# Kernel tuning notes

Hardware: AMD Instinct MI355X
Metric: run time of the kernel (lower is better)

Reference implementation:

```python
import jax, jax.numpy as jnp
import numpy as np

B, L, E, H = 2, 2048, 1024, 16
D = E // H

def setup_inputs() -> dict:
    key = jax.random.key(0)
    ks = jax.random.split(key, 6)
    s = 1.0 / np.sqrt(E)
    return {
        "x": jax.random.normal(ks[0], (B, L, E), dtype=jnp.float32),
        "attention_mask": jnp.ones((B, L), dtype=jnp.float32),
        "Wq": jax.random.normal(ks[1], (E, E), dtype=jnp.float32) * s,
        "Wk": jax.random.normal(ks[2], (E, E), dtype=jnp.float32) * s,
        "Wv": jax.random.normal(ks[3], (E, E), dtype=jnp.float32) * s,
        "Wo": jax.random.normal(ks[4], (E, E), dtype=jnp.float32) * s,
        "bo": jnp.zeros((E,), dtype=jnp.float32),
    }

def reference(x, attention_mask, Wq, Wk, Wv, Wo, bo):
    b, l, e = x.shape
    h, d = H, D

    def proj(W):
        # (B,L,E) @ (E,E)^T -> (B,L,E) -> (B,H,L,D)
        return (x @ W.T).reshape(b, l, h, d).transpose(0, 2, 1, 3)

    q, k, v = proj(Wq), proj(Wk), proj(Wv)

    # multiplicative attention mask on q, k, v (mask shape (B,L) -> (B,1,L,1))
    m = attention_mask[:, None, :, None].astype(x.dtype)
    q, k, v = q * m, k * m, v * m

    scale = 1.0 / np.sqrt(d)
    scores = jnp.einsum('bhqd,bhkd->bhqk', q, k) * scale  # (B,H,L,L)
    causal = jnp.tril(jnp.ones((l, l), dtype=bool))
    scores = jnp.where(causal[None, None], scores, -jnp.inf)
    attn = jax.nn.softmax(scores, axis=-1)
    y = jnp.einsum('bhqk,bhkd->bhqd', attn, v)  # (B,H,L,D)
    y = y.transpose(0, 2, 1, 3).reshape(b, l, e)
    return y @ Wo.T + bo
```

## Files before the change

### kernel.cpp

```cpp
#include <hip/hip_runtime.h>
#include <cstdint>
#include <cstddef>
#include <math.h>

#define BB 2
#define LL 2048
#define EE 1024
#define HH 16
#define DD 64
#define MM (BB*LL)

typedef short short8 __attribute__((ext_vector_type(8)));
typedef float f32x4 __attribute__((ext_vector_type(4)));
typedef float f32x16 __attribute__((ext_vector_type(16)));

#define GPTR __attribute__((address_space(1)))
#define LPTR __attribute__((address_space(3)))

__device__ __forceinline__ unsigned pk_bf16(float lo, float hi) {
  unsigned r;
  asm("v_cvt_pk_bf16_f32 %0, %1, %2" : "=v"(r) : "v"(lo), "v"(hi));
  return r;
}
__device__ __forceinline__ unsigned short f32_bf16(float f) {
  return (unsigned short)pk_bf16(f, f);
}
__device__ __forceinline__ float ex2(float x) {
  float r;
  asm("v_exp_f32 %0, %1" : "=v"(r) : "v"(x));
  return r;
}
__device__ __forceinline__ void swap32(unsigned &a, unsigned &b) {
  asm("v_permlane32_swap_b32 %0, %1" : "+v"(a), "+v"(b));
}
__device__ __forceinline__ float xh_max(float v) {
  union { float f; unsigned u; } a, b;
  a.f = v;
  asm("v_mov_b32 %0, %1" : "=&v"(b.u) : "v"(a.u));
  asm("v_permlane32_swap_b32 %0, %1" : "+v"(a.u), "+v"(b.u));
  return fmaxf(a.f, b.f);
}
__device__ __forceinline__ float xh_sum(float v) {
  union { float f; unsigned u; } a, b;
  a.f = v;
  asm("v_mov_b32 %0, %1" : "=&v"(b.u) : "v"(a.u));
  asm("v_permlane32_swap_b32 %0, %1" : "+v"(a.u), "+v"(b.u));
  return a.f + b.f;
}
__device__ __forceinline__ f32x16 zero16() {
  f32x16 v;
  #pragma unroll
  for (int e = 0; e < 16; ++e) v[e] = 0.f;
  return v;
}

__global__ void cvt_all(const float* __restrict__ x,  const float* __restrict__ wq,
                        const float* __restrict__ wk, const float* __restrict__ wv,
                        const float* __restrict__ wo,
                        unsigned short* __restrict__ xb,  unsigned short* __restrict__ wqb,
                        unsigned short* __restrict__ wkb, unsigned short* __restrict__ wvb,
                        unsigned short* __restrict__ wob)
{
  int i = (blockIdx.x * 256 + threadIdx.x) * 4;
  if (i >= MM * EE + 4 * EE * EE) return;
  const float* s; unsigned short* d; int off;
  if (i < MM * EE) { s = x; d = xb; off = i; }
  else {
    int k = i - MM * EE;
    int w = k >> 20;
    off = k & (EE * EE - 1);
    s = (w == 0) ? wq : (w == 1) ? wk : (w == 2) ? wv : wo;
    d = (w == 0) ? wqb : (w == 1) ? wkb : (w == 2) ? wvb : wob;
  }
  float4 v = *(const float4*)(s + off);
  uint2 o;
  o.x = pk_bf16(v.x, v.y);
  o.y = pk_bf16(v.z, v.w);
  *(uint2*)(d + off) = o;
}

template<int MODE>
__global__ __launch_bounds__(256, 2)
void gemm128(const unsigned short* __restrict__ A,
             const unsigned short* __restrict__ W0,
             const unsigned short* __restrict__ W1,
             const unsigned short* __restrict__ W2,
             const float* __restrict__ mask,
             const float* __restrict__ bias,
             unsigned short* __restrict__ O0,
             unsigned short* __restrict__ O1,
             unsigned short* __restrict__ O2,
             float* __restrict__ OF)
{
  constexpr int K = EE;
  const int tid = threadIdx.x;
  const int lane = tid & 63;
  const int wid = tid >> 6;
  const int g = lane >> 4, li = lane & 15;
  const int m0 = blockIdx.y * 128;
  const int n0 = blockIdx.x * 128;
  const int z = blockIdx.z;

  const unsigned short* Wp = W0;
  if (MODE == 0) Wp = (z == 0) ? W0 : ((z == 1) ? W1 : W2);

  __shared__ unsigned short As[128 * 64];
  __shared__ unsigned short Bs[128 * 64];

  f32x4 acc[4][4];
  f32x4 zero = {0.f, 0.f, 0.f, 0.f};
  #pragma unroll
  for (int i = 0; i < 4; ++i)
    #pragma unroll
    for (int j = 0; j < 4; ++j) acc[i][j] = zero;

  const int wm = (wid >> 1) * 64;
  const int wn = (wid & 1) * 64;

  for (int kt = 0; kt < K; kt += 64) {
    #pragma unroll
    for (int j = 0; j < 4; ++j) {
      int c = j * 256 + tid;
      int row = c >> 3;
      int lcol = ((c & 7) * 16) ^ ((row & 7) << 4);
      __builtin_amdgcn_global_load_lds(
        (const GPTR void*)((const char*)(A + (size_t)(m0 + row) * K + kt) + lcol),
        (LPTR void*)((char*)As + c * 16), 16, 0, 0);
      __builtin_amdgcn_global_load_lds(
        (const GPTR void*)((const char*)(Wp + (size_t)(n0 + row) * K + kt) + lcol),
        (LPTR void*)((char*)Bs + c * 16), 16, 0, 0);
    }
    __syncthreads();

    #pragma unroll
    for (int kk = 0; kk < 2; ++kk) {
      short8 a[4], b[4];
      const int colb = (kk * 32 + g * 8) * 2;
      #pragma unroll
      for (int i = 0; i < 4; ++i) {
        int ar = wm + i * 16 + li;
        a[i] = *(const short8*)((const char*)As + ar * 128 + (colb ^ ((ar & 7) << 4)));
        int br = wn + i * 16 + li;
        b[i] = *(const short8*)((const char*)Bs + br * 128 + (colb ^ ((br & 7) << 4)));
      }
      #pragma unroll
      for (int i = 0; i < 4; ++i)
        #pragma unroll
        for (int j = 0; j < 4; ++j)
          acc[i][j] = __builtin_amdgcn_mfma_f32_16x16x32_bf16(a[i], b[j], acc[i][j], 0, 0, 0);
    }
    __syncthreads();
  }

  if (MODE == 0) {
    if (z == 2) {
      #pragma unroll
      for (int i = 0; i < 4; ++i) {
        int mbase = m0 + wm + i * 16 + g * 4;
        int bb2 = mbase >> 11;
        int l0  = mbase & (LL - 1);
        float mk[4];
        #pragma unroll
        for (int r = 0; r < 4; ++r) mk[r] = mask[mbase + r];
        #pragma unroll
        for (int j = 0; j < 4; ++j) {
          int n = n0 + wn + j * 16 + li;
          int h2 = n >> 6, dd2 = n & 63;
          uint2 o;
          o.x = pk_bf16(acc[i][j][0] * mk[0], acc[i][j][1] * mk[1]);
          o.y = pk_bf16(acc[i][j][2] * mk[2], acc[i][j][3] * mk[3]);
          size_t off = (size_t)(bb2 * HH + h2) * (LL * DD)
                     + (size_t)(l0 >> 5) * (DD * 32) + dd2 * 32 + (l0 & 31);
          *(uint2*)(O2 + off) = o;
        }
      }
    } else {
      unsigned short* Op = (z == 0) ? O0 : O1;
      const float sc = (z == 0) ? 0.125f * 1.44269504088896f : 1.0f;
      #pragma unroll
      for (int i = 0; i < 4; ++i) {
        #pragma unroll
        for (int r = 0; r < 4; ++r) {
          int m = m0 + wm + i * 16 + g * 4 + r;
          float mk = mask[m] * sc;
          int bb = m >> 11;
          int l  = m & (LL - 1);
          #pragma unroll
          for (int j = 0; j < 4; ++j) {
            int n = n0 + wn + j * 16 + li;
            int h = n >> 6, d = n & 63;
            size_t off = (((size_t)(bb * HH + h)) * LL + l) * DD + d;
            Op[off] = f32_bf16(acc[i][j][r] * mk);
          }
        }
      }
    }
  } else {
    #pragma unroll
    for (int i = 0; i < 4; ++i) {
      #pragma unroll
      for (int j = 0; j < 4; ++j) {
        int n = n0 + wn + j * 16 + li;
        float bv = bias[n];
        #pragma unroll
        for (int r = 0; r < 4; ++r) {
          int m = m0 + wm + i * 16 + g * 4 + r;
          OF[(size_t)m * EE + n] = acc[i][j][r] + bv;
        }
      }
    }
  }
}

__global__ __launch_bounds__(128, 2)
void attn11(const unsigned short* __restrict__ Q,
            const unsigned short* __restrict__ K,
            const unsigned short* __restrict__ VT,
            unsigned short* __restrict__ Y)
{
  const int tid = threadIdx.x, lane = tid & 63, w = tid >> 6;
  const int l31 = lane & 31, hi = lane >> 5;

  const int id = blockIdx.x;
  const int lo = id & 7;
  const int r_ = id >> 3;
  const int bh = (r_ & 3) * 8 + lo;
  const int p  = r_ >> 2;
  const int qth = 63 - p;
  const int qtl = p;
  const int b = bh >> 4, h = bh & (HH - 1);
  const size_t kbase = (size_t)bh * LL * DD;

  const unsigned short* Kg  = K + kbase;
  const unsigned short* VTg = VT + kbase;

  const int qrh = qth * 32 + l31;
  const int qrl = qtl * 32 + l31;

  short8 qfh[4], qfl[4];
  {
    const unsigned short* Qr = Q + kbase + (size_t)qrh * DD + hi * 8;
    #pragma unroll
    for (int kc = 0; kc < 4; ++kc) qfh[kc] = *(const short8*)(Qr + kc * 16);
    const unsigned short* Qs = Q + kbase + (size_t)qrl * DD + hi * 8;
    #pragma unroll
    for (int kc = 0; kc < 4; ++kc) qfl[kc] = *(const short8*)(Qs + kc * 16);
  }

  const f32x16 kZero = zero16();
  f32x16 oh0 = zero16(), oh1 = zero16(), ol0 = zero16(), ol1 = zero16();
  float mh = -INFINITY, ml = -INFINITY;
  float lsh4[4] = {0.f, 0.f, 0.f, 0.f};
  float lsl4[4] = {0.f, 0.f, 0.f, 0.f};

  short8 kA[4], vA[4], kB[4], vB[4];

  auto loadtile = [&](short8 (&kk)[4], short8 (&vv)[4], int t2) {
    const int kv0 = t2 << 5;
    const unsigned short* Kp = Kg + ((size_t)(kv0 + l31) << 6) + hi * 8;
    #pragma unroll
    for (int kc = 0; kc < 4; ++kc) kk[kc] = *(const short8*)(Kp + kc * 16);
    const unsigned short* Vp = VTg + (size_t)(kv0 >> 5) * (DD * 32) + l31 * 32 + hi * 8;
    vv[0] = *(const short8*)(Vp);
    vv[1] = *(const short8*)(Vp + 16);
    vv[2] = *(const short8*)(Vp + 32 * 32);
    vv[3] = *(const short8*)(Vp + 32 * 32 + 16);
  };

  loadtile(kA, vA, w);

  auto qk = [&](const short8 (&ck)[4], const short8 (&qf)[4]) -> f32x16 {
    f32x16 s0 = __builtin_amdgcn_mfma_f32_32x32x16_bf16(ck[0], qf[0], kZero, 0, 0, 0);
    f32x16 s1 = __builtin_amdgcn_mfma_f32_32x32x16_bf16(ck[1], qf[1], kZero, 0, 0, 0);
    s0 = __builtin_amdgcn_mfma_f32_32x32x16_bf16(ck[2], qf[2], s0, 0, 0, 0);
    s1 = __builtin_amdgcn_mfma_f32_32x32x16_bf16(ck[3], qf[3], s1, 0, 0, 0);
    #pragma unroll
    for (int e = 0; e < 16; ++e) s0[e] += s1[e];
    return s0;
  };

  auto diagmask = [&](f32x16 &s) {
    #pragma unroll
    for (int i = 0; i < 16; ++i) {
      int kvr = (i & 3) + 8 * (i >> 2) + 4 * hi;
      if (kvr > l31) s[i] = -INFINITY;
    }
  };

  auto process = [&](f32x16 &s, const short8 (&cv)[4],
                     float &mq, float (&ls4)[4], f32x16 &o0, f32x16 &o1) {
    float r0 = fmaxf(fmaxf(fmaxf(s[0], s[8]),  fmaxf(s[1], s[9])),  fmaxf(s[2], s[10]));
    float r1 = fmaxf(fmaxf(fmaxf(s[3], s[11]), fmaxf(s[4], s[12])), fmaxf(s[5], s[13]));
    float r2 = fmaxf(fmaxf(s[6], s[14]), fmaxf(s[7], s[15]));
    float mv = fmaxf(fmaxf(r0, r1), r2);

    if (!__all(mv <= mq + 8.0f)) {
      float mnew = fmaxf(mq, xh_max(mv));
      float al = ex2(mq - mnew);
      mq = mnew;
      #pragma unroll
      for (int e = 0; e < 16; ++e) { o0[e] *= al; o1[e] *= al; }
      #pragma unroll
      for (int e = 0; e < 4; ++e) ls4[e] *= al;
    }

    #pragma unroll
    for (int e = 0; e < 16; ++e) s[e] = ex2(s[e] - mq);
    ls4[0] += (s[0] + s[8])  + (s[4] + s[12]);
    ls4[1] += (s[1] + s[9])  + (s[5] + s[13]);
    ls4[2] += (s[2] + s[10]) + (s[6] + s[14]);
    ls4[3] += (s[3] + s[11]) + (s[7] + s[15]);

    auto mkfrag = [&](int base) -> short8 {
      unsigned a0 = pk_bf16(s[base + 0], s[base + 1]);
      unsigned a1 = pk_bf16(s[base + 2], s[base + 3]);
      unsigned b0 = pk_bf16(s[base + 4], s[base + 5]);
      unsigned b1 = pk_bf16(s[base + 6], s[base + 7]);
      swap32(a0, b0);
      swap32(a1, b1);
      union { unsigned u[4]; short8 s8; } f;
      f.u[0] = a0; f.u[1] = a1; f.u[2] = b0; f.u[3] = b1;
      return f.s8;
    };
    short8 pf0 = mkfrag(0), pf1 = mkfrag(8);

    o0 = __builtin_amdgcn_mfma_f32_32x32x16_bf16(cv[0], pf0, o0, 0, 0, 0);
    o1 = __builtin_amdgcn_mfma_f32_32x32x16_bf16(cv[2], pf0, o1, 0, 0, 0);
    o0 = __builtin_amdgcn_mfma_f32_32x32x16_bf16(cv[1], pf1, o0, 0, 0, 0);
    o1 = __builtin_amdgcn_mfma_f32_32x32x16_bf16(cv[3], pf1, o1, 0, 0, 0);
  };

  auto body = [&](short8 (&ck)[4], short8 (&cv)[4],
                  short8 (&nk)[4], short8 (&nv)[4], int t) {
    if (t + 2 <= qth) loadtile(nk, nv, t + 2);

    if (t <= qtl) {
      f32x16 sh = qk(ck, qfh);
      f32x16 sl = qk(ck, qfl);
      if (t == qtl) diagmask(sl);
      process(sh, cv, mh, lsh4, oh0, oh1);
      process(sl, cv, ml, lsl4, ol0, ol1);
    } else {
      f32x16 sh = qk(ck, qfh);
      if (t == qth) diagmask(sh);
      process(sh, cv, mh, lsh4, oh0, oh1);
    }
  };

  for (int t = w; t <= qth; t += 4) {
    body(kA, vA, kB, vB, t);
    if (t + 2 <= qth) body(kB, vB, kA, vA, t + 2);
  }

  float lsh = (lsh4[0] + lsh4[1]) + (lsh4[2] + lsh4[3]);
  float lsl = (lsl4[0] + lsl4[1]) + (lsl4[2] + lsl4[3]);

  __shared__ float mg[2][64][34];
  if (w == 1) {
    mg[0][lane][0] = mh; mg[0][lane][1] = lsh;
    mg[1][lane][0] = ml; mg[1][lane][1] = lsl;
    #pragma unroll
    for (int e = 0; e < 16; ++e) {
      mg[0][lane][2 + e] = oh0[e]; mg[0][lane][18 + e] = oh1[e];
      mg[1][lane][2 + e] = ol0[e]; mg[1][lane][18 + e] = ol1[e];
    }
  }
  __syncthreads();
  if (w == 0) {
    #pragma unroll
    for (int q = 0; q < 2; ++q) {
      float mw = (q == 0) ? mh : ml;
      float lw = (q == 0) ? lsh : lsl;
      const f32x16& o0 = (q == 0) ? oh0 : ol0;
      const f32x16& o1 = (q == 0) ? oh1 : ol1;
      int qrow = (q == 0) ? qrh : qrl;
      float m1 = mg[q][lane][0], l1 = mg[q][lane][1];
      float M = fmaxf(mw, m1);
      float a0 = ex2(fmaxf(mw - M, -200.0f));
      float a1 = ex2(fmaxf(m1 - M, -200.0f));
      float LtH = lw * a0 + l1 * a1;
      float Lt = xh_sum(LtH);
      float inv = 1.0f / Lt;
      unsigned short* Yr = Y + ((size_t)b * LL + qrow) * EE + h * DD;
      #pragma unroll
      for (int rg = 0; rg < 4; ++rg) {
        uint2 u0, u1;
        int i = rg * 4;
        u0.x = pk_bf16((o0[i]     * a0 + mg[q][lane][2 + i]     * a1) * inv,
                       (o0[i + 1] * a0 + mg[q][lane][3 + i]     * a1) * inv);
        u0.y = pk_bf16((o0[i + 2] * a0 + mg[q][lane][4 + i]     * a1) * inv,
                       (o0[i + 3] * a0 + mg[q][lane][5 + i]     * a1) * inv);
        u1.x = pk_bf16((o1[i]     * a0 + mg[q][lane][18 + i]    * a1) * inv,
                       (o1[i + 1] * a0 + mg[q][lane][19 + i]    * a1) * inv);
        u1.y = pk_bf16((o1[i + 2] * a0 + mg[q][lane][20 + i]    * a1) * inv,
                       (o1[i + 3] * a0 + mg[q][lane][21 + i]    * a1) * inv);
        *(uint2*)(Yr + rg * 8 + hi * 4) = u0;
        *(uint2*)(Yr + 32 + rg * 8 + hi * 4) = u1;
      }
    }
  }
}

extern "C" void kernel_launch(void* const* d_in, const int* in_sizes, int n_in,
                              void* d_out, int out_size, void* d_ws, size_t ws_size,
                              hipStream_t stream) {
  const float* x    = (const float*)d_in[0];
  const float* mask = (const float*)d_in[1];
  const float* Wq   = (const float*)d_in[2];
  const float* Wk   = (const float*)d_in[3];
  const float* Wv   = (const float*)d_in[4];
  const float* Wo   = (const float*)d_in[5];
  const float* bo   = (const float*)d_in[6];
  float* out = (float*)d_out;

  char* ws = (char*)d_ws;
  unsigned short* xb  = (unsigned short*)(ws);
  unsigned short* wqb = (unsigned short*)(ws + ((size_t)8  << 20));
  unsigned short* wkb = (unsigned short*)(ws + ((size_t)10 << 20));
  unsigned short* wvb = (unsigned short*)(ws + ((size_t)12 << 20));
  unsigned short* wob = (unsigned short*)(ws + ((size_t)14 << 20));
  unsigned short* Qb  = (unsigned short*)(ws + ((size_t)16 << 20));
  unsigned short* Kb  = (unsigned short*)(ws + ((size_t)24 << 20));
  unsigned short* VTb = (unsigned short*)(ws + ((size_t)32 << 20));
  unsigned short* Yb  = (unsigned short*)(ws + ((size_t)40 << 20));

  cvt_all<<<8192, 256, 0, stream>>>(x, Wq, Wk, Wv, Wo, xb, wqb, wkb, wvb, wob);

  gemm128<0><<<dim3(EE / 128, MM / 128, 3), 256, 0, stream>>>(
      xb, wqb, wkb, wvb, mask, nullptr, Qb, Kb, VTb, nullptr);

  attn11<<<dim3(1024), 128, 0, stream>>>(Qb, Kb, VTb, Yb);

  gemm128<1><<<dim3(EE / 128, MM / 128, 1), 256, 0, stream>>>(
      Yb, wob, nullptr, nullptr, nullptr, bo, nullptr, nullptr, nullptr, out);
}
```

Measured before the change: 107.5 us.

## Restructure attention loop with split accumulators and paired softmax rescale

The attention kernel's KV loop is restructured so the high query tile keeps two independent online-softmax accumulators, one for even tiles and one for odd tiles. They are merged at the end. Two score tiles are processed together with a single combined rescale vote, and the next tile loads are issued after the current tile is consumed rather than before. The QK product now uses one serial MFMA chain instead of two partial chains plus an add. The aim is more instruction-level parallelism and fewer divergent rescale branches, at the cost of more registers (extra accumulators) and a serial MFMA dependency chain.

```diff
diff --git a/kernel.cpp b/kernel.cpp
--- a/kernel.cpp
+++ b/kernel.cpp
@@ -213,7 +213,7 @@
 }
 
 __global__ __launch_bounds__(128, 2)
-void attn11(const unsigned short* __restrict__ Q,
+void attn12(const unsigned short* __restrict__ Q,
             const unsigned short* __restrict__ K,
             const unsigned short* __restrict__ VT,
             unsigned short* __restrict__ Y)
@@ -247,13 +247,13 @@
     for (int kc = 0; kc < 4; ++kc) qfl[kc] = *(const short8*)(Qs + kc * 16);
   }
 
-  const f32x16 kZero = zero16();
-  f32x16 oh0 = zero16(), oh1 = zero16(), ol0 = zero16(), ol1 = zero16();
-  float mh = -INFINITY, ml = -INFINITY;
-  float lsh4[4] = {0.f, 0.f, 0.f, 0.f};
-  float lsl4[4] = {0.f, 0.f, 0.f, 0.f};
-
-  short8 kA[4], vA[4], kB[4], vB[4];
+  f32x16 oE0 = zero16(), oE1 = zero16();
+  f32x16 oO0 = zero16(), oO1 = zero16();
+  f32x16 oL0 = zero16(), oL1 = zero16();
+  float mE = -INFINITY, mO = -INFINITY, mL = -INFINITY;
+  float lsE0 = 0.f, lsE1 = 0.f, lsO0 = 0.f, lsO1 = 0.f, lsL0 = 0.f, lsL1 = 0.f;
+
+  short8 kE[4], vE[4], kO[4], vO[4];
 
   auto loadtile = [&](short8 (&kk)[4], short8 (&vv)[4], int t2) {
     const int kv0 = t2 << 5;
@@ -267,16 +267,12 @@
     vv[3] = *(const short8*)(Vp + 32 * 32 + 16);
   };
 
-  loadtile(kA, vA, w);
-
-  auto qk = [&](const short8 (&ck)[4], const short8 (&qf)[4]) -> f32x16 {
-    f32x16 s0 = __builtin_amdgcn_mfma_f32_32x32x16_bf16(ck[0], qf[0], kZero, 0, 0, 0);
-    f32x16 s1 = __builtin_amdgcn_mfma_f32_32x32x16_bf16(ck[1], qf[1], kZero, 0, 0, 0);
-    s0 = __builtin_amdgcn_mfma_f32_32x32x16_bf16(ck[2], qf[2], s0, 0, 0, 0);
-    s1 = __builtin_amdgcn_mfma_f32_32x32x16_bf16(ck[3], qf[3], s1, 0, 0, 0);
-    #pragma unroll
-    for (int e = 0; e < 16; ++e) s0[e] += s1[e];
-    return s0;
+  auto qk4 = [&](const short8 (&ck)[4], const short8 (&qf)[4]) -> f32x16 {
+    f32x16 s = __builtin_amdgcn_mfma_f32_32x32x16_bf16(ck[0], qf[0], zero16(), 0, 0, 0);
+    s = __builtin_amdgcn_mfma_f32_32x32x16_bf16(ck[1], qf[1], s, 0, 0, 0);
+    s = __builtin_amdgcn_mfma_f32_32x32x16_bf16(ck[2], qf[2], s, 0, 0, 0);
+    s = __builtin_amdgcn_mfma_f32_32x32x16_bf16(ck[3], qf[3], s, 0, 0, 0);
+    return s;
   };
 
   auto diagmask = [&](f32x16 &s) {
@@ -287,92 +283,151 @@
     }
   };
 
-  auto process = [&](f32x16 &s, const short8 (&cv)[4],
-                     float &mq, float (&ls4)[4], f32x16 &o0, f32x16 &o1) {
+  auto localmax = [&](const f32x16 &s) -> float {
     float r0 = fmaxf(fmaxf(fmaxf(s[0], s[8]),  fmaxf(s[1], s[9])),  fmaxf(s[2], s[10]));
     float r1 = fmaxf(fmaxf(fmaxf(s[3], s[11]), fmaxf(s[4], s[12])), fmaxf(s[5], s[13]));
     float r2 = fmaxf(fmaxf(s[6], s[14]), fmaxf(s[7], s[15]));
-    float mv = fmaxf(fmaxf(r0, r1), r2);
-
-    if (!__all(mv <= mq + 8.0f)) {
-      float mnew = fmaxf(mq, xh_max(mv));
-      float al = ex2(mq - mnew);
-      mq = mnew;
-      #pragma unroll
-      for (int e = 0; e < 16; ++e) { o0[e] *= al; o1[e] *= al; }
-      #pragma unroll
-      for (int e = 0; e < 4; ++e) ls4[e] *= al;
-    }
-
+    return fmaxf(fmaxf(r0, r1), r2);
+  };
+
+  auto mkfrag = [&](const f32x16 &s, int base) -> short8 {
+    unsigned a0 = pk_bf16(s[base + 0], s[base + 1]);
+    unsigned a1 = pk_bf16(s[base + 2], s[base + 3]);
+    unsigned b0 = pk_bf16(s[base + 4], s[base + 5]);
+    unsigned b1 = pk_bf16(s[base + 6], s[base + 7]);
+    swap32(a0, b0);
+    swap32(a1, b1);
+    union { unsigned u[4]; short8 s8; } f;
+    f.u[0] = a0; f.u[1] = a1; f.u[2] = b0; f.u[3] = b1;
+    return f.s8;
+  };
+
+  auto tail = [&](f32x16 &s, float mq, float &l0, float &l1,
+                  const short8 (&cv)[4], f32x16 &o0, f32x16 &o1) {
     #pragma unroll
     for (int e = 0; e < 16; ++e) s[e] = ex2(s[e] - mq);
-    ls4[0] += (s[0] + s[8])  + (s[4] + s[12]);
-    ls4[1] += (s[1] + s[9])  + (s[5] + s[13]);
-    ls4[2] += (s[2] + s[10]) + (s[6] + s[14]);
-    ls4[3] += (s[3] + s[11]) + (s[7] + s[15]);
-
-    auto mkfrag = [&](int base) -> short8 {
-      unsigned a0 = pk_bf16(s[base + 0], s[base + 1]);
-      unsigned a1 = pk_bf16(s[base + 2], s[base + 3]);
-      unsigned b0 = pk_bf16(s[base + 4], s[base + 5]);
-      unsigned b1 = pk_bf16(s[base + 6], s[base + 7]);
-      swap32(a0, b0);
-      swap32(a1, b1);
-      union { unsigned u[4]; short8 s8; } f;
-      f.u[0] = a0; f.u[1] = a1; f.u[2] = b0; f.u[3] = b1;
-      return f.s8;
-    };
-    short8 pf0 = mkfrag(0), pf1 = mkfrag(8);
-
+    l0 += (s[0] + s[8])  + (s[4] + s[12]) + (s[1] + s[9])  + (s[5] + s[13]);
+    l1 += (s[2] + s[10]) + (s[6] + s[14]) + (s[3] + s[11]) + (s[7] + s[15]);
+    short8 pf0 = mkfrag(s, 0), pf1 = mkfrag(s, 8);
     o0 = __builtin_amdgcn_mfma_f32_32x32x16_bf16(cv[0], pf0, o0, 0, 0, 0);
     o1 = __builtin_amdgcn_mfma_f32_32x32x16_bf16(cv[2], pf0, o1, 0, 0, 0);
     o0 = __builtin_amdgcn_mfma_f32_32x32x16_bf16(cv[1], pf1, o0, 0, 0, 0);
     o1 = __builtin_amdgcn_mfma_f32_32x32x16_bf16(cv[3], pf1, o1, 0, 0, 0);
   };
 
-  auto body = [&](short8 (&ck)[4], short8 (&cv)[4],
-                  short8 (&nk)[4], short8 (&nv)[4], int t) {
-    if (t + 2 <= qth) loadtile(nk, nv, t + 2);
-
+  auto pp = [&](f32x16 &sA, float &mA, float &lA0, float &lA1,
+                const short8 (&cvA)[4], f32x16 &a0, f32x16 &a1,
+                f32x16 &sB, float &mB, float &lB0, float &lB1,
+                const short8 (&cvB)[4], f32x16 &b0, f32x16 &b1) {
+    float mvA = localmax(sA);
+    float mvB = localmax(sB);
+    if (!__all(fmaxf(mvA - mA, mvB - mB) <= 8.0f)) {
+      float mnA = fmaxf(mA, xh_max(mvA));
+      float alA = ex2(mA - mnA);
+      mA = mnA; lA0 *= alA; lA1 *= alA;
+      #pragma unroll
+      for (int e = 0; e < 16; ++e) { a0[e] *= alA; a1[e] *= alA; }
+      float mnB = fmaxf(mB, xh_max(mvB));
+      float alB = ex2(mB - mnB);
+      mB = mnB; lB0 *= alB; lB1 *= alB;
+      #pragma unroll
+      for (int e = 0; e < 16; ++e) { b0[e] *= alB; b1[e] *= alB; }
+    }
+    tail(sA, mA, lA0, lA1, cvA, a0, a1);
+    tail(sB, mB, lB0, lB1, cvB, b0, b1);
+  };
+
+  auto ps = [&](f32x16 &s, float &mq, float &l0, float &l1,
+                const short8 (&cv)[4], f32x16 &o0, f32x16 &o1) {
+    float mv = localmax(s);
+    if (!__all(mv <= mq + 8.0f)) {
+      float mn = fmaxf(mq, xh_max(mv));
+      float al = ex2(mq - mn);
+      mq = mn; l0 *= al; l1 *= al;
+      #pragma unroll
+      for (int e = 0; e < 16; ++e) { o0[e] *= al; o1[e] *= al; }
+    }
+    tail(s, mq, l0, l1, cv, o0, o1);
+  };
+
+  loadtile(kE, vE, w);
+  loadtile(kO, vO, w + 2);
+
+  int t = w;
+  while (t + 2 <= qth) {
+    const bool shE = (t <= qtl), shO = (t + 2 <= qtl);
+    if (shE) {
+      f32x16 sE = qk4(kE, qfh);
+      f32x16 sL = qk4(kE, qfl);
+      if (t == qtl) diagmask(sL);
+      pp(sE, mE, lsE0, lsE1, vE, oE0, oE1,
+         sL, mL, lsL0, lsL1, vE, oL0, oL1);
+      if (t + 4 <= qth) loadtile(kE, vE, t + 4);
+      f32x16 sO = qk4(kO, qfh);
+      if (shO) {
+        f32x16 sL2 = qk4(kO, qfl);
+        if (t + 2 == qtl) diagmask(sL2);
+        pp(sO, mO, lsO0, lsO1, vO, oO0, oO1,
+           sL2, mL, lsL0, lsL1, vO, oL0, oL1);
+      } else {
+        if (t + 2 == qth) diagmask(sO);
+        ps(sO, mO, lsO0, lsO1, vO, oO0, oO1);
+      }
+      if (t + 6 <= qth) loadtile(kO, vO, t + 6);
+    } else {
+      f32x16 sE = qk4(kE, qfh);
+      f32x16 sO = qk4(kO, qfh);
+      if (t + 2 == qth) diagmask(sO);
+      pp(sE, mE, lsE0, lsE1, vE, oE0, oE1,
+         sO, mO, lsO0, lsO1, vO, oO0, oO1);
+      if (t + 4 <= qth) loadtile(kE, vE, t + 4);
+      if (t + 6 <= qth) loadtile(kO, vO, t + 6);
+    }
+    t += 4;
+  }
+  if (t <= qth) {
+    f32x16 sE = qk4(kE, qfh);
+    if (t == qth) diagmask(sE);
     if (t <= qtl) {
-      f32x16 sh = qk(ck, qfh);
-      f32x16 sl = qk(ck, qfl);
-      if (t == qtl) diagmask(sl);
-      process(sh, cv, mh, lsh4, oh0, oh1);
-      process(sl, cv, ml, lsl4, ol0, ol1);
+      f32x16 sL = qk4(kE, qfl);
+      if (t == qtl) diagmask(sL);
+      pp(sE, mE, lsE0, lsE1, vE, oE0, oE1,
+         sL, mL, lsL0, lsL1, vE, oL0, oL1);
     } else {
-      f32x16 sh = qk(ck, qfh);
-      if (t == qth) diagmask(sh);
-      process(sh, cv, mh, lsh4, oh0, oh1);
-    }
-  };
-
-  for (int t = w; t <= qth; t += 4) {
-    body(kA, vA, kB, vB, t);
-    if (t + 2 <= qth) body(kB, vB, kA, vA, t + 2);
-  }
-
-  float lsh = (lsh4[0] + lsh4[1]) + (lsh4[2] + lsh4[3]);
-  float lsl = (lsl4[0] + lsl4[1]) + (lsl4[2] + lsl4[3]);
+      ps(sE, mE, lsE0, lsE1, vE, oE0, oE1);
+    }
+  }
+
+  float mH = fmaxf(mE, mO);
+  float aE = ex2(fmaxf(mE - mH, -200.0f));
+  float aO = ex2(fmaxf(mO - mH, -200.0f));
+  float lsH = (lsE0 + lsE1) * aE + (lsO0 + lsO1) * aO;
+  f32x16 oh0, oh1;
+  #pragma unroll
+  for (int e = 0; e < 16; ++e) {
+    oh0[e] = oE0[e] * aE + oO0[e] * aO;
+    oh1[e] = oE1[e] * aE + oO1[e] * aO;
+  }
+  float lsL = lsL0 + lsL1;
 
   __shared__ float mg[2][64][34];
   if (w == 1) {
-    mg[0][lane][0] = mh; mg[0][lane][1] = lsh;
-    mg[1][lane][0] = ml; mg[1][lane][1] = lsl;
+    mg[0][lane][0] = mH; mg[0][lane][1] = lsH;
+    mg[1][lane][0] = mL; mg[1][lane][1] = lsL;
     #pragma unroll
     for (int e = 0; e < 16; ++e) {
       mg[0][lane][2 + e] = oh0[e]; mg[0][lane][18 + e] = oh1[e];
-      mg[1][lane][2 + e] = ol0[e]; mg[1][lane][18 + e] = ol1[e];
+      mg[1][lane][2 + e] = oL0[e]; mg[1][lane][18 + e] = oL1[e];
     }
   }
   __syncthreads();
   if (w == 0) {
     #pragma unroll
     for (int q = 0; q < 2; ++q) {
-      float mw = (q == 0) ? mh : ml;
-      float lw = (q == 0) ? lsh : lsl;
-      const f32x16& o0 = (q == 0) ? oh0 : ol0;
-      const f32x16& o1 = (q == 0) ? oh1 : ol1;
+      float mw = (q == 0) ? mH : mL;
+      float lw = (q == 0) ? lsH : lsL;
+      const f32x16& o0 = (q == 0) ? oh0 : oL0;
+      const f32x16& o1 = (q == 0) ? oh1 : oL1;
       int qrow = (q == 0) ? qrh : qrl;
       float m1 = mg[q][lane][0], l1 = mg[q][lane][1];
       float M = fmaxf(mw, m1);
@@ -386,14 +441,14 @@
       for (int rg = 0; rg < 4; ++rg) {
         uint2 u0, u1;
         int i = rg * 4;
-        u0.x = pk_bf16((o0[i]     * a0 + mg[q][lane][2 + i]     * a1) * inv,
-                       (o0[i + 1] * a0 + mg[q][lane][3 + i]     * a1) * inv);
-        u0.y = pk_bf16((o0[i + 2] * a0 + mg[q][lane][4 + i]     * a1) * inv,
-                       (o0[i + 3] * a0 + mg[q][lane][5 + i]     * a1) * inv);
-        u1.x = pk_bf16((o1[i]     * a0 + mg[q][lane][18 + i]    * a1) * inv,
-                       (o1[i + 1] * a0 + mg[q][lane][19 + i]    * a1) * inv);
-        u1.y = pk_bf16((o1[i + 2] * a0 + mg[q][lane][20 + i]    * a1) * inv,
-                       (o1[i + 3] * a0 + mg[q][lane][21 + i]    * a1) * inv);
+        u0.x = pk_bf16((o0[i]     * a0 + mg[q][lane][2 + i]  * a1) * inv,
+                       (o0[i + 1] * a0 + mg[q][lane][3 + i]  * a1) * inv);
+        u0.y = pk_bf16((o0[i + 2] * a0 + mg[q][lane][4 + i]  * a1) * inv,
+                       (o0[i + 3] * a0 + mg[q][lane][5 + i]  * a1) * inv);
+        u1.x = pk_bf16((o1[i]     * a0 + mg[q][lane][18 + i] * a1) * inv,
+                       (o1[i + 1] * a0 + mg[q][lane][19 + i] * a1) * inv);
+        u1.y = pk_bf16((o1[i + 2] * a0 + mg[q][lane][20 + i] * a1) * inv,
+                       (o1[i + 3] * a0 + mg[q][lane][21 + i] * a1) * inv);
         *(uint2*)(Yr + rg * 8 + hi * 4) = u0;
         *(uint2*)(Yr + 32 + rg * 8 + hi * 4) = u1;
       }
@@ -429,7 +484,7 @@
   gemm128<0><<<dim3(EE / 128, MM / 128, 3), 256, 0, stream>>>(
       xb, wqb, wkb, wvb, mask, nullptr, Qb, Kb, VTb, nullptr);
 
-  attn11<<<dim3(1024), 128, 0, stream>>>(Qb, Kb, VTb, Yb);
+  attn12<<<dim3(1024), 128, 0, stream>>>(Qb, Kb, VTb, Yb);
 
   gemm128<1><<<dim3(EE / 128, MM / 128, 1), 256, 0, stream>>>(
       Yb, wob, nullptr, nullptr, nullptr, bo, nullptr, nullptr, nullptr, out);
```

After: 112.4 us. 4.6% more time.

## Double-buffer LDS tiles in projection GEMMs and flatten QKV grid

Applied to the files above, without the earlier changes.

The projection GEMM now ping-pongs between two LDS buffers. The next K-tile's global-to-LDS loads are issued before the MFMAs on the current tile, so load latency overlaps compute and one barrier per iteration is removed. The QKV launch becomes a flat 2D grid that treats the contiguous Wq/Wk/Wv bf16 copies as a single 3072-row weight matrix and derives the output selector from n0. LDS use per block doubles to 64KB, which may limit occupancy. The merged grid depends on the three weight buffers staying adjacent in the workspace.

```diff
diff --git a/kernel.cpp b/kernel.cpp
--- a/kernel.cpp
+++ b/kernel.cpp
@@ -81,16 +81,14 @@
 
 template<int MODE>
 __global__ __launch_bounds__(256, 2)
-void gemm128(const unsigned short* __restrict__ A,
-             const unsigned short* __restrict__ W0,
-             const unsigned short* __restrict__ W1,
-             const unsigned short* __restrict__ W2,
-             const float* __restrict__ mask,
-             const float* __restrict__ bias,
-             unsigned short* __restrict__ O0,
-             unsigned short* __restrict__ O1,
-             unsigned short* __restrict__ O2,
-             float* __restrict__ OF)
+void gemm2p(const unsigned short* __restrict__ A,
+            const unsigned short* __restrict__ W,
+            const float* __restrict__ mask,
+            const float* __restrict__ bias,
+            unsigned short* __restrict__ O0,
+            unsigned short* __restrict__ O1,
+            unsigned short* __restrict__ O2,
+            float* __restrict__ OF)
 {
   constexpr int K = EE;
   const int tid = threadIdx.x;
@@ -99,13 +97,9 @@
   const int g = lane >> 4, li = lane & 15;
   const int m0 = blockIdx.y * 128;
   const int n0 = blockIdx.x * 128;
-  const int z = blockIdx.z;
-
-  const unsigned short* Wp = W0;
-  if (MODE == 0) Wp = (z == 0) ? W0 : ((z == 1) ? W1 : W2);
-
-  __shared__ unsigned short As[128 * 64];
-  __shared__ unsigned short Bs[128 * 64];
+
+  __shared__ unsigned short As[2][128 * 64];
+  __shared__ unsigned short Bs[2][128 * 64];
 
   f32x4 acc[4][4];
   f32x4 zero = {0.f, 0.f, 0.f, 0.f};
@@ -117,7 +111,7 @@
   const int wm = (wid >> 1) * 64;
   const int wn = (wid & 1) * 64;
 
-  for (int kt = 0; kt < K; kt += 64) {
+  auto stage = [&](int buf, int kt) {
     #pragma unroll
     for (int j = 0; j < 4; ++j) {
       int c = j * 256 + tid;
@@ -125,12 +119,20 @@
       int lcol = ((c & 7) * 16) ^ ((row & 7) << 4);
       __builtin_amdgcn_global_load_lds(
         (const GPTR void*)((const char*)(A + (size_t)(m0 + row) * K + kt) + lcol),
-        (LPTR void*)((char*)As + c * 16), 16, 0, 0);
+        (LPTR void*)((char*)As[buf] + c * 16), 16, 0, 0);
       __builtin_amdgcn_global_load_lds(
-        (const GPTR void*)((const char*)(Wp + (size_t)(n0 + row) * K + kt) + lcol),
-        (LPTR void*)((char*)Bs + c * 16), 16, 0, 0);
-    }
-    __syncthreads();
+        (const GPTR void*)((const char*)(W + (size_t)(n0 + row) * K + kt) + lcol),
+        (LPTR void*)((char*)Bs[buf] + c * 16), 16, 0, 0);
+    }
+  };
+
+  stage(0, 0);
+  asm volatile("s_waitcnt vmcnt(0)" ::: "memory");
+  __builtin_amdgcn_s_barrier();
+
+  int cur = 0;
+  for (int kt = 0; kt < K; kt += 64) {
+    if (kt + 64 < K) stage(cur ^ 1, kt + 64);
 
     #pragma unroll
     for (int kk = 0; kk < 2; ++kk) {
@@ -139,9 +141,9 @@
       #pragma unroll
       for (int i = 0; i < 4; ++i) {
         int ar = wm + i * 16 + li;
-        a[i] = *(const short8*)((const char*)As + ar * 128 + (colb ^ ((ar & 7) << 4)));
+        a[i] = *(const short8*)((const char*)As[cur] + ar * 128 + (colb ^ ((ar & 7) << 4)));
         int br = wn + i * 16 + li;
-        b[i] = *(const short8*)((const char*)Bs + br * 128 + (colb ^ ((br & 7) << 4)));
+        b[i] = *(const short8*)((const char*)Bs[cur] + br * 128 + (colb ^ ((br & 7) << 4)));
       }
       #pragma unroll
       for (int i = 0; i < 4; ++i)
@@ -149,10 +151,16 @@
         for (int j = 0; j < 4; ++j)
           acc[i][j] = __builtin_amdgcn_mfma_f32_16x16x32_bf16(a[i], b[j], acc[i][j], 0, 0, 0);
     }
-    __syncthreads();
+
+    if (kt + 64 < K) {
+      asm volatile("s_waitcnt vmcnt(0) lgkmcnt(0)" ::: "memory");
+      __builtin_amdgcn_s_barrier();
+      cur ^= 1;
+    }
   }
 
   if (MODE == 0) {
+    const int z = n0 >> 10;
     if (z == 2) {
       #pragma unroll
       for (int i = 0; i < 4; ++i) {
@@ -164,7 +172,7 @@
         for (int r = 0; r < 4; ++r) mk[r] = mask[mbase + r];
         #pragma unroll
         for (int j = 0; j < 4; ++j) {
-          int n = n0 + wn + j * 16 + li;
+          int n = (n0 & 1023) + wn + j * 16 + li;
           int h2 = n >> 6, dd2 = n & 63;
           uint2 o;
           o.x = pk_bf16(acc[i][j][0] * mk[0], acc[i][j][1] * mk[1]);
@@ -187,7 +195,7 @@
           int l  = m & (LL - 1);
           #pragma unroll
           for (int j = 0; j < 4; ++j) {
-            int n = n0 + wn + j * 16 + li;
+            int n = (n0 & 1023) + wn + j * 16 + li;
             int h = n >> 6, d = n & 63;
             size_t off = (((size_t)(bb * HH + h)) * LL + l) * DD + d;
             Op[off] = f32_bf16(acc[i][j][r] * mk);
@@ -426,11 +434,11 @@
 
   cvt_all<<<8192, 256, 0, stream>>>(x, Wq, Wk, Wv, Wo, xb, wqb, wkb, wvb, wob);
 
-  gemm128<0><<<dim3(EE / 128, MM / 128, 3), 256, 0, stream>>>(
-      xb, wqb, wkb, wvb, mask, nullptr, Qb, Kb, VTb, nullptr);
+  gemm2p<0><<<dim3(3 * EE / 128, MM / 128), 256, 0, stream>>>(
+      xb, wqb, mask, nullptr, Qb, Kb, VTb, nullptr);
 
   attn11<<<dim3(1024), 128, 0, stream>>>(Qb, Kb, VTb, Yb);
 
-  gemm128<1><<<dim3(EE / 128, MM / 128, 1), 256, 0, stream>>>(
-      Yb, wob, nullptr, nullptr, nullptr, bo, nullptr, nullptr, nullptr, out);
-}
+  gemm2p<1><<<dim3(EE / 128, MM / 128), 256, 0, stream>>>(
+      Yb, wob, nullptr, bo, nullptr, nullptr, nullptr, out);
+}
```

Measured after the change: 115.0 us. 7.0% more time.

## Split paired query tiles into one tile per block with higher occupancy

Applied to the files above, without the earlier changes.

The attention kernel used to handle a heavy and a light causal query tile per block, with a double-buffered K/V register prefetch. Now each block processes a single query tile, the grid doubles to 2048 blocks, and launch bounds allow 4 blocks per CU. The aim is to cut register pressure and rely on occupancy rather than explicit prefetch to hide memory latency. In exchange it drops the software prefetch and the K/V reuse across the two tiles, so K/V loads double and the causal workload becomes uneven across blocks, with heavy tiles scheduled first.

```diff
diff --git a/kernel.cpp b/kernel.cpp
--- a/kernel.cpp
+++ b/kernel.cpp
@@ -212,8 +212,8 @@
   }
 }
 
-__global__ __launch_bounds__(128, 2)
-void attn11(const unsigned short* __restrict__ Q,
+__global__ __launch_bounds__(128, 4)
+void attn13(const unsigned short* __restrict__ Q,
             const unsigned short* __restrict__ K,
             const unsigned short* __restrict__ VT,
             unsigned short* __restrict__ Y)
@@ -225,70 +225,61 @@
   const int lo = id & 7;
   const int r_ = id >> 3;
   const int bh = (r_ & 3) * 8 + lo;
-  const int p  = r_ >> 2;
-  const int qth = 63 - p;
-  const int qtl = p;
+  const int qt = 63 - (r_ >> 2);
   const int b = bh >> 4, h = bh & (HH - 1);
   const size_t kbase = (size_t)bh * LL * DD;
 
   const unsigned short* Kg  = K + kbase;
   const unsigned short* VTg = VT + kbase;
 
-  const int qrh = qth * 32 + l31;
-  const int qrl = qtl * 32 + l31;
-
-  short8 qfh[4], qfl[4];
+  const int qrow = qt * 32 + l31;
+
+  short8 qf[4];
   {
-    const unsigned short* Qr = Q + kbase + (size_t)qrh * DD + hi * 8;
-    #pragma unroll
-    for (int kc = 0; kc < 4; ++kc) qfh[kc] = *(const short8*)(Qr + kc * 16);
-    const unsigned short* Qs = Q + kbase + (size_t)qrl * DD + hi * 8;
-    #pragma unroll
-    for (int kc = 0; kc < 4; ++kc) qfl[kc] = *(const short8*)(Qs + kc * 16);
+    const unsigned short* Qr = Q + kbase + (size_t)qrow * DD + hi * 8;
+    #pragma unroll
+    for (int kc = 0; kc < 4; ++kc) qf[kc] = *(const short8*)(Qr + kc * 16);
   }
 
   const f32x16 kZero = zero16();
-  f32x16 oh0 = zero16(), oh1 = zero16(), ol0 = zero16(), ol1 = zero16();
-  float mh = -INFINITY, ml = -INFINITY;
-  float lsh4[4] = {0.f, 0.f, 0.f, 0.f};
-  float lsl4[4] = {0.f, 0.f, 0.f, 0.f};
-
-  short8 kA[4], vA[4], kB[4], vB[4];
-
-  auto loadtile = [&](short8 (&kk)[4], short8 (&vv)[4], int t2) {
-    const int kv0 = t2 << 5;
-    const unsigned short* Kp = Kg + ((size_t)(kv0 + l31) << 6) + hi * 8;
-    #pragma unroll
-    for (int kc = 0; kc < 4; ++kc) kk[kc] = *(const short8*)(Kp + kc * 16);
-    const unsigned short* Vp = VTg + (size_t)(kv0 >> 5) * (DD * 32) + l31 * 32 + hi * 8;
-    vv[0] = *(const short8*)(Vp);
-    vv[1] = *(const short8*)(Vp + 16);
-    vv[2] = *(const short8*)(Vp + 32 * 32);
-    vv[3] = *(const short8*)(Vp + 32 * 32 + 16);
-  };
-
-  loadtile(kA, vA, w);
-
-  auto qk = [&](const short8 (&ck)[4], const short8 (&qf)[4]) -> f32x16 {
-    f32x16 s0 = __builtin_amdgcn_mfma_f32_32x32x16_bf16(ck[0], qf[0], kZero, 0, 0, 0);
-    f32x16 s1 = __builtin_amdgcn_mfma_f32_32x32x16_bf16(ck[1], qf[1], kZero, 0, 0, 0);
-    s0 = __builtin_amdgcn_mfma_f32_32x32x16_bf16(ck[2], qf[2], s0, 0, 0, 0);
-    s1 = __builtin_amdgcn_mfma_f32_32x32x16_bf16(ck[3], qf[3], s1, 0, 0, 0);
-    #pragma unroll
-    for (int e = 0; e < 16; ++e) s0[e] += s1[e];
-    return s0;
-  };
-
-  auto diagmask = [&](f32x16 &s) {
-    #pragma unroll
-    for (int i = 0; i < 16; ++i) {
-      int kvr = (i & 3) + 8 * (i >> 2) + 4 * hi;
-      if (kvr > l31) s[i] = -INFINITY;
-    }
-  };
-
-  auto process = [&](f32x16 &s, const short8 (&cv)[4],
-                     float &mq, float (&ls4)[4], f32x16 &o0, f32x16 &o1) {
+  f32x16 o0 = zero16(), o1 = zero16();
+  float mq = -INFINITY;
+  float ls4[4] = {0.f, 0.f, 0.f, 0.f};
+
+  short8 kA[4], vA[4];
+
+  for (int t = w; t <= qt; t += 2) {
+    {
+      const int kv0 = t << 5;
+      const unsigned short* Kp = Kg + ((size_t)(kv0 + l31) << 6) + hi * 8;
+      #pragma unroll
+      for (int kc = 0; kc < 4; ++kc) kA[kc] = *(const short8*)(Kp + kc * 16);
+      const unsigned short* Vp = VTg + (size_t)(kv0 >> 5) * (DD * 32) + l31 * 32 + hi * 8;
+      vA[0] = *(const short8*)(Vp);
+      vA[1] = *(const short8*)(Vp + 16);
+      vA[2] = *(const short8*)(Vp + 32 * 32);
+      vA[3] = *(const short8*)(Vp + 32 * 32 + 16);
+    }
+
+    f32x16 s;
+    {
+      f32x16 s0 = __builtin_amdgcn_mfma_f32_32x32x16_bf16(kA[0], qf[0], kZero, 0, 0, 0);
+      f32x16 s1 = __builtin_amdgcn_mfma_f32_32x32x16_bf16(kA[1], qf[1], kZero, 0, 0, 0);
+      s0 = __builtin_amdgcn_mfma_f32_32x32x16_bf16(kA[2], qf[2], s0, 0, 0, 0);
+      s1 = __builtin_amdgcn_mfma_f32_32x32x16_bf16(kA[3], qf[3], s1, 0, 0, 0);
+      #pragma unroll
+      for (int e = 0; e < 16; ++e) s0[e] += s1[e];
+      s = s0;
+    }
+
+    if (t == qt) {
+      #pragma unroll
+      for (int i = 0; i < 16; ++i) {
+        int kvr = (i & 3) + 8 * (i >> 2) + 4 * hi;
+        if (kvr > l31) s[i] = -INFINITY;
+      }
+    }
+
     float r0 = fmaxf(fmaxf(fmaxf(s[0], s[8]),  fmaxf(s[1], s[9])),  fmaxf(s[2], s[10]));
     float r1 = fmaxf(fmaxf(fmaxf(s[3], s[11]), fmaxf(s[4], s[12])), fmaxf(s[5], s[13]));
     float r2 = fmaxf(fmaxf(s[6], s[14]), fmaxf(s[7], s[15]));
@@ -324,79 +315,46 @@
     };
     short8 pf0 = mkfrag(0), pf1 = mkfrag(8);
 
-    o0 = __builtin_amdgcn_mfma_f32_32x32x16_bf16(cv[0], pf0, o0, 0, 0, 0);
-    o1 = __builtin_amdgcn_mfma_f32_32x32x16_bf16(cv[2], pf0, o1, 0, 0, 0);
-    o0 = __builtin_amdgcn_mfma_f32_32x32x16_bf16(cv[1], pf1, o0, 0, 0, 0);
-    o1 = __builtin_amdgcn_mfma_f32_32x32x16_bf16(cv[3], pf1, o1, 0, 0, 0);
-  };
-
-  auto body = [&](short8 (&ck)[4], short8 (&cv)[4],
-                  short8 (&nk)[4], short8 (&nv)[4], int t) {
-    if (t + 2 <= qth) loadtile(nk, nv, t + 2);
-
-    if (t <= qtl) {
-      f32x16 sh = qk(ck, qfh);
-      f32x16 sl = qk(ck, qfl);
-      if (t == qtl) diagmask(sl);
-      process(sh, cv, mh, lsh4, oh0, oh1);
-      process(sl, cv, ml, lsl4, ol0, ol1);
-    } else {
-      f32x16 sh = qk(ck, qfh);
-      if (t == qth) diagmask(sh);
-      process(sh, cv, mh, lsh4, oh0, oh1);
-    }
-  };
-
-  for (int t = w; t <= qth; t += 4) {
-    body(kA, vA, kB, vB, t);
-    if (t + 2 <= qth) body(kB, vB, kA, vA, t + 2);
-  }
-
-  float lsh = (lsh4[0] + lsh4[1]) + (lsh4[2] + lsh4[3]);
-  float lsl = (lsl4[0] + lsl4[1]) + (lsl4[2] + lsl4[3]);
-
-  __shared__ float mg[2][64][34];
+    o0 = __builtin_amdgcn_mfma_f32_32x32x16_bf16(vA[0], pf0, o0, 0, 0, 0);
+    o1 = __builtin_amdgcn_mfma_f32_32x32x16_bf16(vA[2], pf0, o1, 0, 0, 0);
+    o0 = __builtin_amdgcn_mfma_f32_32x32x16_bf16(vA[1], pf1, o0, 0, 0, 0);
+    o1 = __builtin_amdgcn_mfma_f32_32x32x16_bf16(vA[3], pf1, o1, 0, 0, 0);
+  }
+
+  float lq = (ls4[0] + ls4[1]) + (ls4[2] + ls4[3]);
+
+  __shared__ float mg[64][34];
   if (w == 1) {
-    mg[0][lane][0] = mh; mg[0][lane][1] = lsh;
-    mg[1][lane][0] = ml; mg[1][lane][1] = lsl;
+    mg[lane][0] = mq; mg[lane][1] = lq;
     #pragma unroll
     for (int e = 0; e < 16; ++e) {
-      mg[0][lane][2 + e] = oh0[e]; mg[0][lane][18 + e] = oh1[e];
-      mg[1][lane][2 + e] = ol0[e]; mg[1][lane][18 + e] = ol1[e];
+      mg[lane][2 + e] = o0[e]; mg[lane][18 + e] = o1[e];
     }
   }
   __syncthreads();
   if (w == 0) {
-    #pragma unroll
-    for (int q = 0; q < 2; ++q) {
-      float mw = (q == 0) ? mh : ml;
-      float lw = (q == 0) ? lsh : lsl;
-      const f32x16& o0 = (q == 0) ? oh0 : ol0;
-      const f32x16& o1 = (q == 0) ? oh1 : ol1;
-      int qrow = (q == 0) ? qrh : qrl;
-      float m1 = mg[q][lane][0], l1 = mg[q][lane][1];
-      float M = fmaxf(mw, m1);
-      float a0 = ex2(fmaxf(mw - M, -200.0f));
-      float a1 = ex2(fmaxf(m1 - M, -200.0f));
-      float LtH = lw * a0 + l1 * a1;
-      float Lt = xh_sum(LtH);
-      float inv = 1.0f / Lt;
-      unsigned short* Yr = Y + ((size_t)b * LL + qrow) * EE + h * DD;
-      #pragma unroll
-      for (int rg = 0; rg < 4; ++rg) {
-        uint2 u0, u1;
-        int i = rg * 4;
-        u0.x = pk_bf16((o0[i]     * a0 + mg[q][lane][2 + i]     * a1) * inv,
-                       (o0[i + 1] * a0 + mg[q][lane][3 + i]     * a1) * inv);
-        u0.y = pk_bf16((o0[i + 2] * a0 + mg[q][lane][4 + i]     * a1) * inv,
-                       (o0[i + 3] * a0 + mg[q][lane][5 + i]     * a1) * inv);
-        u1.x = pk_bf16((o1[i]     * a0 + mg[q][lane][18 + i]    * a1) * inv,
-                       (o1[i + 1] * a0 + mg[q][lane][19 + i]    * a1) * inv);
-        u1.y = pk_bf16((o1[i + 2] * a0 + mg[q][lane][20 + i]    * a1) * inv,
-                       (o1[i + 3] * a0 + mg[q][lane][21 + i]    * a1) * inv);
-        *(uint2*)(Yr + rg * 8 + hi * 4) = u0;
-        *(uint2*)(Yr + 32 + rg * 8 + hi * 4) = u1;
-      }
+    float m1 = mg[lane][0], l1 = mg[lane][1];
+    float M = fmaxf(mq, m1);
+    float a0 = ex2(fmaxf(mq - M, -200.0f));
+    float a1 = ex2(fmaxf(m1 - M, -200.0f));
+    float LtH = lq * a0 + l1 * a1;
+    float Lt = xh_sum(LtH);
+    float inv = 1.0f / Lt;
+    unsigned short* Yr = Y + ((size_t)b * LL + qrow) * EE + h * DD;
+    #pragma unroll
+    for (int rg = 0; rg < 4; ++rg) {
+      uint2 u0, u1;
+      int i = rg * 4;
+      u0.x = pk_bf16((o0[i]     * a0 + mg[lane][2 + i]  * a1) * inv,
+                     (o0[i + 1] * a0 + mg[lane][3 + i]  * a1) * inv);
+      u0.y = pk_bf16((o0[i + 2] * a0 + mg[lane][4 + i]  * a1) * inv,
+                     (o0[i + 3] * a0 + mg[lane][5 + i]  * a1) * inv);
+      u1.x = pk_bf16((o1[i]     * a0 + mg[lane][18 + i] * a1) * inv,
+                     (o1[i + 1] * a0 + mg[lane][19 + i] * a1) * inv);
+      u1.y = pk_bf16((o1[i + 2] * a0 + mg[lane][20 + i] * a1) * inv,
+                     (o1[i + 3] * a0 + mg[lane][21 + i] * a1) * inv);
+      *(uint2*)(Yr + rg * 8 + hi * 4) = u0;
+      *(uint2*)(Yr + 32 + rg * 8 + hi * 4) = u1;
     }
   }
 }
@@ -429,7 +387,7 @@
   gemm128<0><<<dim3(EE / 128, MM / 128, 3), 256, 0, stream>>>(
       xb, wqb, wkb, wvb, mask, nullptr, Qb, Kb, VTb, nullptr);
 
-  attn11<<<dim3(1024), 128, 0, stream>>>(Qb, Kb, VTb, Yb);
+  attn13<<<dim3(2048), 128, 0, stream>>>(Qb, Kb, VTb, Yb);
 
   gemm128<1><<<dim3(EE / 128, MM / 128, 1), 256, 0, stream>>>(
       Yb, wob, nullptr, nullptr, nullptr, bo, nullptr, nullptr, nullptr, out);
```

New measurement: 119.8 us. 1.11x slower.
